# Kernel tuning notes

Measured on AMD Instinct MI355X. Metric: run time of the kernel, lower is better.

The kernel has to match this reference:

```python
import jax, jax.numpy as jnp
import numpy as np
import math

N_HEADS = 16
ROPE_BASE = 10000.0


def _rope_interleaved(t, cos, sin):
    # t: [B,H,T,dk]; cos/sin: [T, dk//2] broadcast over B,H
    te, to = t[..., 0::2], t[..., 1::2]
    re = te * cos - to * sin
    ro = te * sin + to * cos
    # interleave back: [..., dk//2, 2] -> [..., dk]
    return jnp.stack([re, ro], axis=-1).reshape(t.shape)


def setup_inputs() -> dict:
    key = jax.random.key(0)
    ks = jax.random.split(key, 5)
    B, T, C = 2, 2048, 1024
    s = 1.0 / math.sqrt(C)
    return {
        "x": jax.random.normal(ks[0], (B, T, C), dtype=jnp.float32),
        "W_qkv": jax.random.normal(ks[1], (C, 3 * C), dtype=jnp.float32) * s,
        "b_qkv": jax.random.normal(ks[2], (3 * C,), dtype=jnp.float32) * 0.02,
        "W_proj": jax.random.normal(ks[3], (C, C), dtype=jnp.float32) * s,
        "b_proj": jax.random.normal(ks[4], (C,), dtype=jnp.float32) * 0.02,
    }


def reference(x, W_qkv, b_qkv, W_proj, b_proj):
    B, T, C = x.shape
    H = N_HEADS
    dk = C // H

    qkv = x @ W_qkv + b_qkv                      # [B,T,3C]
    q, k, v = jnp.split(qkv, 3, axis=-1)
    q = q.reshape(B, T, H, dk).transpose(0, 2, 1, 3)  # [B,H,T,dk]
    k = k.reshape(B, T, H, dk).transpose(0, 2, 1, 3)
    v = v.reshape(B, T, H, dk).transpose(0, 2, 1, 3)

    # RoPE angles: pos * base^(-2i/dk)
    freqs = ROPE_BASE ** (-2.0 * jnp.arange(dk // 2, dtype=jnp.float32) / dk)
    angles = jnp.arange(T, dtype=jnp.float32)[:, None] * freqs[None, :]  # [T,dk//2]
    cos, sin = jnp.cos(angles), jnp.sin(angles)

    q = _rope_interleaved(q, cos, sin)
    k = _rope_interleaved(k, cos, sin)

    attn = jnp.einsum("bhqd,bhkd->bhqk", q, k) / math.sqrt(dk)  # [B,H,T,T]
    causal = jnp.triu(jnp.full((T, T), -jnp.inf, dtype=attn.dtype), k=1)
    attn = jax.nn.softmax(attn + causal, axis=-1)

    scores = jnp.einsum("bhqk,bhkd->bhqd", attn, v)  # [B,H,T,dk]
    scores = scores.transpose(0, 2, 1, 3).reshape(B, T, C)
    return scores @ W_proj + b_proj
```

## Files before the change

### kernel.cpp

```cpp
#include <hip/hip_runtime.h>
#include <hip/hip_bf16.h>

typedef __bf16 bf16x8 __attribute__((ext_vector_type(8)));
typedef float f32x4 __attribute__((ext_vector_type(4)));
typedef float f32x16 __attribute__((ext_vector_type(16)));
typedef unsigned short u16;
typedef u16 u16x8 __attribute__((ext_vector_type(8)));

__device__ __forceinline__ u16 f2bf(float f) {
  union { float f; unsigned u; } v; v.f = f;
  unsigned r = v.u + 0x7fffu + ((v.u >> 16) & 1u);
  return (u16)(r >> 16);
}
__device__ __forceinline__ float bf2f(u16 u) {
  union { unsigned u; float f; } v; v.u = (unsigned)u << 16; return v.f;
}
__device__ __forceinline__ unsigned cvtpk(float a, float b) {
  unsigned r;
  asm("v_cvt_pk_bf16_f32 %0, %1, %2" : "=v"(r) : "v"(a), "v"(b));
  return r;
}
__device__ __forceinline__ float exp2_(float x) {
  float r;
  asm("v_exp_f32 %0, %1" : "=v"(r) : "v"(x));
  return r;
}
__device__ __forceinline__ float sin2pi_(float x) {
  float r;
  asm("v_sin_f32 %0, %1" : "=v"(r) : "v"(x));
  return r;
}
__device__ __forceinline__ float cos2pi_(float x) {
  float r;
  asm("v_cos_f32 %0, %1" : "=v"(r) : "v"(x));
  return r;
}
__device__ __forceinline__ void gload16(const void* g, void* l) {
  __builtin_amdgcn_global_load_lds(
      (__attribute__((address_space(1))) void*)(void*)g,
      (__attribute__((address_space(3))) void*)l, 16, 0, 0);
}

union U8 { bf16x8 v; unsigned u[4]; };

__global__ __launch_bounds__(256) void cast_x_k(const float* __restrict__ x,
                                                u16* __restrict__ xb, int n8) {
  int id = blockIdx.x * 256 + threadIdx.x;
  if (id >= n8) return;
  const float4* p = (const float4*)(x + (size_t)id * 8);
  float4 a = p[0], b = p[1];
  u16x8 o;
  o[0] = f2bf(a.x); o[1] = f2bf(a.y); o[2] = f2bf(a.z); o[3] = f2bf(a.w);
  o[4] = f2bf(b.x); o[5] = f2bf(b.y); o[6] = f2bf(b.z); o[7] = f2bf(b.w);
  *(u16x8*)(xb + (size_t)id * 8) = o;
}

__global__ __launch_bounds__(256) void tcast_k(const float* __restrict__ W,
                                               u16* __restrict__ Wt, int R, int Cc) {
  __shared__ float tile[32][33];
  int bx = blockIdx.x * 32, by = blockIdx.y * 32;
  int tx = threadIdx.x & 31, ty = threadIdx.x >> 5;
#pragma unroll
  for (int j = 0; j < 4; j++)
    tile[ty + j * 8][tx] = W[(size_t)(by + ty + j * 8) * Cc + bx + tx];
  __syncthreads();
#pragma unroll
  for (int j = 0; j < 4; j++)
    Wt[(size_t)(bx + ty + j * 8) * R + by + tx] = f2bf(tile[tx][ty + j * 8]);
}

template <bool BF16OUT>
__global__ __launch_bounds__(256) void gemm_bt_k(const u16* __restrict__ A,
                                                 const u16* __restrict__ Bt,
                                                 const float* __restrict__ bias,
                                                 void* __restrict__ Cv,
                                                 int M, int N, int K) {
  __shared__ u16 As[128 * 64];
  __shared__ u16 Bs[128 * 64];
  int tid = threadIdx.x;
  int m0 = blockIdx.y * 128, n0 = blockIdx.x * 128;
  int wave = tid >> 6, lane = tid & 63;
  int wm = (wave & 1) * 64, wn = (wave >> 1) * 64;
  int lrow = lane & 15, lk = (lane >> 4) * 8;
  int rr = lane >> 3, cb = (lane & 7) * 16;

  f32x4 acc[4][4] = {};

  for (int k0 = 0; k0 < K; k0 += 64) {
#pragma unroll
    for (int i = 0; i < 4; i++) {
      int row = wave * 32 + i * 8 + rr;
      int cc = (cb ^ ((row & 7) << 4)) >> 1;
      gload16(A + (size_t)(m0 + row) * K + k0 + cc, &As[(wave * 32 + i * 8) * 64]);
      gload16(Bt + (size_t)(n0 + row) * K + k0 + cc, &Bs[(wave * 32 + i * 8) * 64]);
    }
    __syncthreads();
#pragma unroll
    for (int kk = 0; kk < 2; kk++) {
      bf16x8 af[4], bfr[4];
#pragma unroll
      for (int i = 0; i < 4; i++) {
        int arow = wm + i * 16 + lrow;
        int ab = (arow * 128 + (kk * 32 + lk) * 2) ^ ((arow & 7) << 4);
        af[i] = *(const bf16x8*)((const char*)As + ab);
        int brow = wn + i * 16 + lrow;
        int bb = (brow * 128 + (kk * 32 + lk) * 2) ^ ((brow & 7) << 4);
        bfr[i] = *(const bf16x8*)((const char*)Bs + bb);
      }
#pragma unroll
      for (int i = 0; i < 4; i++)
#pragma unroll
        for (int j = 0; j < 4; j++)
          acc[i][j] = __builtin_amdgcn_mfma_f32_16x16x32_bf16(af[i], bfr[j], acc[i][j], 0, 0, 0);
    }
    __syncthreads();
  }
  int rg = lane >> 4;
#pragma unroll
  for (int i = 0; i < 4; i++) {
#pragma unroll
    for (int j = 0; j < 4; j++) {
      int col = n0 + wn + j * 16 + lrow;
      float bz = bias ? bias[col] : 0.f;
#pragma unroll
      for (int r = 0; r < 4; r++) {
        int row = m0 + wm + i * 16 + rg * 4 + r;
        float val = acc[i][j][r] + bz;
        if constexpr (BF16OUT)
          ((u16*)Cv)[(size_t)row * N + col] = f2bf(val);
        else
          ((float*)Cv)[(size_t)row * N + col] = val;
      }
    }
  }
}

__global__ __launch_bounds__(256) void rope_pack_k(const u16* __restrict__ qkv,
                                                   u16* __restrict__ qf,
                                                   u16* __restrict__ kf,
                                                   u16* __restrict__ vf) {
  __shared__ u16 tl[64][72];
  int bh = blockIdx.x, tb = blockIdx.y;
  int b = bh >> 4, h = bh & 15;
  int tid = threadIdx.x;
  int tloc = tid >> 2;
  int a = tid & 3;
  int tg = tb * 64 + tloc;
  const u16* rowp = qkv + ((size_t)(b * 2048 + tg)) * 3072 + h * 64 + 16 * a;
  u16x8 q0 = *(const u16x8*)(rowp);
  u16x8 q1 = *(const u16x8*)(rowp + 8);
  u16x8 k0 = *(const u16x8*)(rowp + 1024);
  u16x8 k1 = *(const u16x8*)(rowp + 1032);
  const float QS = 0.18033688011112042f;
  const float C1 = -0.41524101186092029f;
  const float C2 = 0.15915494309189535f;
  u16x8 qo0, qo1, ko0, ko1;
#pragma unroll
  for (int j = 0; j < 8; j++) {
    int i = 8 * a + j;
    float fr = (float)tg * (exp2f((float)i * C1) * C2);
    fr = fr - floorf(fr);
    float sv = sin2pi_(fr), cv = cos2pi_(fr);
    float qx, qy, kx, ky;
    if (j < 4) {
      qx = bf2f(q0[2 * j]); qy = bf2f(q0[2 * j + 1]);
      kx = bf2f(k0[2 * j]); ky = bf2f(k0[2 * j + 1]);
    } else {
      qx = bf2f(q1[2 * j - 8]); qy = bf2f(q1[2 * j - 7]);
      kx = bf2f(k1[2 * j - 8]); ky = bf2f(k1[2 * j - 7]);
    }
    u16 qre = f2bf((qx * cv - qy * sv) * QS), qro = f2bf((qx * sv + qy * cv) * QS);
    u16 kre = f2bf(kx * cv - ky * sv),        kro = f2bf(kx * sv + ky * cv);
    if (j < 4) { qo0[2 * j] = qre; qo0[2 * j + 1] = qro; ko0[2 * j] = kre; ko0[2 * j + 1] = kro; }
    else       { qo1[2 * j - 8] = qre; qo1[2 * j - 7] = qro; ko1[2 * j - 8] = kre; ko1[2 * j - 7] = kro; }
  }
  size_t qbase = ((size_t)bh * 64 + (tg >> 5)) * 2048 + a * 512 + (tg & 31) * 8;
  *(u16x8*)(qf + qbase) = qo0;
  *(u16x8*)(qf + qbase + 256) = qo1;
  size_t kbase = (((size_t)bh * 32 + (tg >> 6)) * 2 + ((tg >> 5) & 1)) * 2048 + a * 512 + (tg & 31) * 8;
  *(u16x8*)(kf + kbase) = ko0;
  *(u16x8*)(kf + kbase + 256) = ko1;
#pragma unroll
  for (int rep = 0; rep < 2; rep++) {
    int tr = rep * 32 + (tid >> 3);
    int dc = (tid & 7) * 8;
    u16x8 v = *(const u16x8*)(qkv + ((size_t)(b * 2048 + tb * 64 + tr)) * 3072 + 2048 + h * 64 + dc);
    *(u16x8*)&tl[tr][dc] = v;
  }
  __syncthreads();
  u16* dst = vf + ((size_t)bh * 32 + tb) * 4096;
#pragma unroll
  for (int rep = 0; rep < 2; rep++) {
    int c = rep * 256 + tid;
    int dh = c >> 8, s = (c >> 6) & 3, l = c & 63;
    int hi = l >> 5, ql = l & 31;
    u16x8 o;
#pragma unroll
    for (int j = 0; j < 8; j++) o[j] = tl[s * 16 + hi * 8 + j][dh * 32 + ql];
    *(u16x8*)(dst + (size_t)c * 8) = o;
  }
}


#define KPREF(K0, K1, IT)                                                         \
  do {                                                                            \
    const u16* kb_ = KfP + (size_t)(IT) * 4096 + ln8;                             \
    _Pragma("unroll") for (int d_ = 0; d_ < 4; d_++) {                            \
      K0[d_] = *(const bf16x8*)(kb_ + d_ * 512);                                  \
      K1[d_] = *(const bf16x8*)(kb_ + 2048 + d_ * 512);                           \
    }                                                                             \
  } while (0)

#define QKC(SA, SB, K0, K1)                                                       \
  do {                                                                            \
    SA = (f32x16){};                                                              \
    SB = (f32x16){};                                                              \
    _Pragma("unroll") for (int d_ = 0; d_ < 4; d_++) {                            \
      SA = __builtin_amdgcn_mfma_f32_32x32x16_bf16(K0[d_], qfr[d_], SA, 0, 0, 0); \
      SB = __builtin_amdgcn_mfma_f32_32x32x16_bf16(K1[d_], qfr[d_], SB, 0, 0, 0); \
    }                                                                             \
  } while (0)

#define VLOADM(IT)                                                                \
  do {                                                                            \
    const u16* vb_ = VfP + (size_t)(IT) * 4096 + ln8;                             \
    _Pragma("unroll") for (int s_ = 0; s_ < 4; s_++) {                            \
      vv0[s_] = *(const bf16x8*)(vb_ + s_ * 512);                                 \
      vv1[s_] = *(const bf16x8*)(vb_ + 2048 + s_ * 512);                          \
    }                                                                             \
  } while (0)

#define SMPV(SA, SB, IT, MASKF)                                                   \
  do {                                                                            \
    if (MASKF) {                                                                  \
      int kv0_ = (IT) * 64;                                                       \
      _Pragma("unroll") for (int r_ = 0; r_ < 16; r_++) {                         \
        int ro_ = (r_ & 3) + 8 * (r_ >> 2) + 4 * hi;                              \
        if (kv0_ + ro_ > qg) SA[r_] = -3e38f;                                     \
        if (kv0_ + 32 + ro_ > qg) SB[r_] = -3e38f;                                \
      }                                                                           \
    }                                                                             \
    _Pragma("unroll") for (int r_ = 0; r_ < 16; r_++) {                           \
      SA[r_] = exp2_(SA[r_]);                                                     \
      SB[r_] = exp2_(SB[r_]);                                                     \
    }                                                                             \
    unsigned w0_ = cvtpk(SA[0], SA[1]),   w1_ = cvtpk(SA[2], SA[3]);              \
    unsigned w2_ = cvtpk(SA[4], SA[5]),   w3_ = cvtpk(SA[6], SA[7]);              \
    unsigned w4_ = cvtpk(SA[8], SA[9]),   w5_ = cvtpk(SA[10], SA[11]);            \
    unsigned w6_ = cvtpk(SA[12], SA[13]), w7_ = cvtpk(SA[14], SA[15]);            \
    unsigned y0_ = cvtpk(SB[0], SB[1]),   y1_ = cvtpk(SB[2], SB[3]);              \
    unsigned y2_ = cvtpk(SB[4], SB[5]),   y3_ = cvtpk(SB[6], SB[7]);              \
    unsigned y4_ = cvtpk(SB[8], SB[9]),   y5_ = cvtpk(SB[10], SB[11]);            \
    unsigned y6_ = cvtpk(SB[12], SB[13]), y7_ = cvtpk(SB[14], SB[15]);            \
    asm("v_permlane32_swap_b32 %0, %1" : "+v"(w0_), "+v"(w2_));                   \
    asm("v_permlane32_swap_b32 %0, %1" : "+v"(w1_), "+v"(w3_));                   \
    asm("v_permlane32_swap_b32 %0, %1" : "+v"(w4_), "+v"(w6_));                   \
    asm("v_permlane32_swap_b32 %0, %1" : "+v"(w5_), "+v"(w7_));                   \
    asm("v_permlane32_swap_b32 %0, %1" : "+v"(y0_), "+v"(y2_));                   \
    asm("v_permlane32_swap_b32 %0, %1" : "+v"(y1_), "+v"(y3_));                   \
    asm("v_permlane32_swap_b32 %0, %1" : "+v"(y4_), "+v"(y6_));                   \
    asm("v_permlane32_swap_b32 %0, %1" : "+v"(y5_), "+v"(y7_));                   \
    U8 pf0_, pf1_, pf2_, pf3_;                                                    \
    pf0_.u[0] = w0_; pf0_.u[1] = w1_; pf0_.u[2] = w2_; pf0_.u[3] = w3_;           \
    pf1_.u[0] = w4_; pf1_.u[1] = w5_; pf1_.u[2] = w6_; pf1_.u[3] = w7_;           \
    pf2_.u[0] = y0_; pf2_.u[1] = y1_; pf2_.u[2] = y2_; pf2_.u[3] = y3_;           \
    pf3_.u[0] = y4_; pf3_.u[1] = y5_; pf3_.u[2] = y6_; pf3_.u[3] = y7_;           \
    o0 = __builtin_amdgcn_mfma_f32_32x32x16_bf16(vv0[0], pf0_.v, o0, 0, 0, 0);    \
    o1 = __builtin_amdgcn_mfma_f32_32x32x16_bf16(vv1[0], pf0_.v, o1, 0, 0, 0);    \
    o0 = __builtin_amdgcn_mfma_f32_32x32x16_bf16(vv0[1], pf1_.v, o0, 0, 0, 0);    \
    o1 = __builtin_amdgcn_mfma_f32_32x32x16_bf16(vv1[1], pf1_.v, o1, 0, 0, 0);    \
    o0 = __builtin_amdgcn_mfma_f32_32x32x16_bf16(vv0[2], pf2_.v, o0, 0, 0, 0);    \
    o1 = __builtin_amdgcn_mfma_f32_32x32x16_bf16(vv1[2], pf2_.v, o1, 0, 0, 0);    \
    o0 = __builtin_amdgcn_mfma_f32_32x32x16_bf16(vv0[3], pf3_.v, o0, 0, 0, 0);    \
    o1 = __builtin_amdgcn_mfma_f32_32x32x16_bf16(vv1[3], pf3_.v, o1, 0, 0, 0);    \
    ls = __builtin_amdgcn_mfma_f32_32x32x16_bf16(onesf.v, pf0_.v, ls, 0, 0, 0);   \
    ls = __builtin_amdgcn_mfma_f32_32x32x16_bf16(onesf.v, pf1_.v, ls, 0, 0, 0);   \
    ls = __builtin_amdgcn_mfma_f32_32x32x16_bf16(onesf.v, pf2_.v, ls, 0, 0, 0);   \
    ls = __builtin_amdgcn_mfma_f32_32x32x16_bf16(onesf.v, pf3_.v, ls, 0, 0, 0);   \
  } while (0)

__global__ __launch_bounds__(64) void attn_k(const u16* __restrict__ Qf,
                                             const u16* __restrict__ Kf,
                                             const u16* __restrict__ Vf,
                                             u16* __restrict__ sc,
                                             u16* __restrict__ pO,
                                             float* __restrict__ pL) {
  const int T = 2048;
  int blk = blockIdx.x;
  int bh = (blk & 7) * 4 + ((blk >> 3) & 3);
  int c = blk >> 5;
  int qt, slot, nslots;
  if (c < 32) { qt = 63 - (c >> 1); slot = c & 1; nslots = 2; }
  else        { qt = 79 - c;        slot = 0;     nslots = 1; }
  int nTot = (qt >> 1) + 1;
  int it0 = (nTot * slot) / nslots;
  int itEnd = (nTot * (slot + 1)) / nslots;
  int lane = threadIdx.x & 63;
  int ql = lane & 31, hi = lane >> 5;
  int ln8 = lane * 8;
  int qg = qt * 32 + ql;
  const u16* QfP = Qf + (size_t)bh * 64 * 2048;
  const u16* KfP = Kf + (size_t)bh * 32 * 4096;
  const u16* VfP = Vf + (size_t)bh * 32 * 4096;
  int b = bh >> 4, h = bh & 15;

  U8 onesf;
#pragma unroll
  for (int j = 0; j < 4; j++) onesf.u[j] = 0x3F803F80u;

  bf16x8 qfr[4];
#pragma unroll
  for (int ds = 0; ds < 4; ds++)
    qfr[ds] = *(const bf16x8*)(QfP + (size_t)qt * 2048 + ds * 512 + ln8);

  f32x16 o0 = {}, o1 = {}, ls = {};
  bf16x8 Ka0[4], Ka1[4], Kb0[4], Kb1[4], vv0[4], vv1[4];
  f32x16 sA0, sA1, sB0, sB1;

  int t = it0;
  KPREF(Ka0, Ka1, t);
  QKC(sA0, sA1, Ka0, Ka1);
  if (t + 1 < itEnd) KPREF(Kb0, Kb1, t + 1);

  for (;;) {
    bool last = (t == itEnd - 1);
    VLOADM(t);
    if (t + 2 < itEnd) KPREF(Ka0, Ka1, t + 2);
    if (!last) QKC(sB0, sB1, Kb0, Kb1);
    SMPV(sA0, sA1, t, t == nTot - 1);
    if (last) break;
    ++t;
    last = (t == itEnd - 1);
    VLOADM(t);
    if (t + 2 < itEnd) KPREF(Kb0, Kb1, t + 2);
    if (!last) QKC(sA0, sA1, Ka0, Ka1);
    SMPV(sB0, sB1, t, t == nTot - 1);
    if (last) break;
    ++t;
  }

  if (nslots == 1) {
    float inv = 1.f / ls[0];
    u16* orow = sc + ((size_t)(b * T + qg)) * 1024 + h * 64;
#pragma unroll
    for (int j = 0; j < 4; j++) {
      ushort4 o;
      o.x = f2bf(o0[4 * j + 0] * inv); o.y = f2bf(o0[4 * j + 1] * inv);
      o.z = f2bf(o0[4 * j + 2] * inv); o.w = f2bf(o0[4 * j + 3] * inv);
      *(ushort4*)(orow + 8 * j + 4 * hi) = o;
      ushort4 q2;
      q2.x = f2bf(o1[4 * j + 0] * inv); q2.y = f2bf(o1[4 * j + 1] * inv);
      q2.z = f2bf(o1[4 * j + 2] * inv); q2.w = f2bf(o1[4 * j + 3] * inv);
      *(ushort4*)(orow + 32 + 8 * j + 4 * hi) = q2;
    }
  } else {
    u16* orow = pO + (size_t)slot * 4194304 + ((size_t)(b * T + qg)) * 1024 + h * 64;
#pragma unroll
    for (int j = 0; j < 4; j++) {
      ushort4 o;
      o.x = f2bf(o0[4 * j + 0]); o.y = f2bf(o0[4 * j + 1]);
      o.z = f2bf(o0[4 * j + 2]); o.w = f2bf(o0[4 * j + 3]);
      *(ushort4*)(orow + 8 * j + 4 * hi) = o;
      ushort4 q2;
      q2.x = f2bf(o1[4 * j + 0]); q2.y = f2bf(o1[4 * j + 1]);
      q2.z = f2bf(o1[4 * j + 2]); q2.w = f2bf(o1[4 * j + 3]);
      *(ushort4*)(orow + 32 + 8 * j + 4 * hi) = q2;
    }
    if (hi == 0) pL[slot * 65536 + bh * 2048 + qg] = ls[0];
  }
}

__global__ __launch_bounds__(256) void mrg_k(const u16* __restrict__ pO,
                                             const float* __restrict__ pL,
                                             u16* __restrict__ sc) {
  int id = blockIdx.x * 256 + threadIdx.x;
  int col8 = id & 127;
  int rp = id >> 7;
  int b = rp >> 9;
  int t = 1536 + (rp & 511);
  int h = col8 >> 3;
  int bh = b * 16 + h;
  size_t idx8 = ((size_t)(b * 2048 + t) * 128 + col8);
  float l0 = pL[bh * 2048 + t];
  float l1 = pL[65536 + bh * 2048 + t];
  u16x8 v0 = *(const u16x8*)(pO + idx8 * 8);
  u16x8 v1 = *(const u16x8*)(pO + 4194304 + idx8 * 8);
  float inv = 1.f / (l0 + l1);
  u16x8 o;
#pragma unroll
  for (int j = 0; j < 8; j++) o[j] = f2bf((bf2f(v0[j]) + bf2f(v1[j])) * inv);
  *(u16x8*)(sc + idx8 * 8) = o;
}

extern "C" void kernel_launch(void* const* d_in, const int* in_sizes, int n_in,
                              void* d_out, int out_size, void* d_ws, size_t ws_size,
                              hipStream_t stream) {
  const float* x      = (const float*)d_in[0];
  const float* W_qkv  = (const float*)d_in[1];
  const float* b_qkv  = (const float*)d_in[2];
  const float* W_proj = (const float*)d_in[3];
  const float* b_proj = (const float*)d_in[4];
  float* out = (float*)d_out;

  const int B = 2, T = 2048, C = 1024;
  const int M = B * T;

  char* ws = (char*)d_ws;
  u16* wprojt = (u16*)(ws);
  u16* xb     = (u16*)(ws + (2ull << 20));
  u16* wqkvt  = (u16*)(ws + (10ull << 20));
  u16* qkvb   = (u16*)(ws + (16ull << 20));
  u16* pO     = (u16*)(ws + (2ull << 20));
  float* pL   = (float*)(ws + (34ull << 20));
  u16* qfb    = (u16*)(ws + (40ull << 20));
  u16* kfb    = (u16*)(ws + (48ull << 20));
  u16* vfb    = (u16*)(ws + (56ull << 20));
  u16* sc     = (u16*)(ws + (64ull << 20));

  cast_x_k<<<(M * C / 8 + 255) / 256, 256, 0, stream>>>(x, xb, M * C / 8);
  tcast_k<<<dim3(3 * C / 32, C / 32), 256, 0, stream>>>(W_qkv, wqkvt, C, 3 * C);
  tcast_k<<<dim3(C / 32, C / 32), 256, 0, stream>>>(W_proj, wprojt, C, C);
  gemm_bt_k<true><<<dim3(3 * C / 128, M / 128), 256, 0, stream>>>(xb, wqkvt, b_qkv, qkvb, M, 3 * C, C);
  rope_pack_k<<<dim3(B * 16, T / 64), 256, 0, stream>>>(qkvb, qfb, kfb, vfb);
  attn_k<<<2560, 64, 0, stream>>>(qfb, kfb, vfb, sc, pO, pL);
  mrg_k<<<512, 256, 0, stream>>>(pO, pL, sc);
  gemm_bt_k<false><<<dim3(C / 128, M / 128), 256, 0, stream>>>(sc, wprojt, b_proj, out, M, C, C);
}
```

Before: 118.5 us.

## Fuse RoPE and Q/K/V repacking into QKV GEMM epilogue, merge weight casts

The QKV GEMM epilogue now applies bias, RoPE (using a precomputed cos/sin table and lane shuffles to pair even/odd columns) and writes Q, K, V directly in the attention kernel's packed layouts. This removes the bf16 qkv intermediate buffer and the separate rope_pack kernel. The two weight transpose-cast launches are merged into one kernel, and a small table kernel is added. In exchange, the epilogue issues scattered 2-byte stores and per-element table loads, which may be less coalesced than the old packing pass.

```diff
diff --git a/kernel.cpp b/kernel.cpp
--- a/kernel.cpp
+++ b/kernel.cpp
@@ -42,6 +42,16 @@
 }
 
 union U8 { bf16x8 v; unsigned u[4]; };
+
+__global__ __launch_bounds__(256) void ctab_k(float2* __restrict__ ctab) {
+  int id = blockIdx.x * 256 + threadIdx.x;
+  int t = id >> 5, i = id & 31;
+  const float C1 = -0.41524101186092029f;
+  const float C2 = 0.15915494309189535f;
+  float fr = (float)t * (exp2f((float)i * C1) * C2);
+  fr = fr - floorf(fr);
+  ctab[id] = make_float2(cos2pi_(fr), sin2pi_(fr));
+}
 
 __global__ __launch_bounds__(256) void cast_x_k(const float* __restrict__ x,
                                                 u16* __restrict__ xb, int n8) {
@@ -55,10 +65,17 @@
   *(u16x8*)(xb + (size_t)id * 8) = o;
 }
 
-__global__ __launch_bounds__(256) void tcast_k(const float* __restrict__ W,
-                                               u16* __restrict__ Wt, int R, int Cc) {
+__global__ __launch_bounds__(256) void tcast2_k(const float* __restrict__ Wq,
+                                                const float* __restrict__ Wp,
+                                                u16* __restrict__ Wqt,
+                                                u16* __restrict__ Wpt) {
   __shared__ float tile[32][33];
-  int bx = blockIdx.x * 32, by = blockIdx.y * 32;
+  int bxr = blockIdx.x;
+  const float* W; u16* Wt; int Cc, bx;
+  if (bxr < 96) { W = Wq; Wt = Wqt; Cc = 3072; bx = bxr * 32; }
+  else          { W = Wp; Wt = Wpt; Cc = 1024; bx = (bxr - 96) * 32; }
+  const int R = 1024;
+  int by = blockIdx.y * 32;
   int tx = threadIdx.x & 31, ty = threadIdx.x >> 5;
 #pragma unroll
   for (int j = 0; j < 4; j++)
@@ -135,72 +152,105 @@
   }
 }
 
-__global__ __launch_bounds__(256) void rope_pack_k(const u16* __restrict__ qkv,
+__global__ __launch_bounds__(256) void gemm_qkvf_k(const u16* __restrict__ A,
+                                                   const u16* __restrict__ Bt,
+                                                   const float* __restrict__ bias,
+                                                   const float2* __restrict__ ctab,
                                                    u16* __restrict__ qf,
                                                    u16* __restrict__ kf,
                                                    u16* __restrict__ vf) {
-  __shared__ u16 tl[64][72];
-  int bh = blockIdx.x, tb = blockIdx.y;
-  int b = bh >> 4, h = bh & 15;
+  const int K = 1024;
+  __shared__ u16 As[128 * 64];
+  __shared__ u16 Bs[128 * 64];
   int tid = threadIdx.x;
-  int tloc = tid >> 2;
-  int a = tid & 3;
-  int tg = tb * 64 + tloc;
-  const u16* rowp = qkv + ((size_t)(b * 2048 + tg)) * 3072 + h * 64 + 16 * a;
-  u16x8 q0 = *(const u16x8*)(rowp);
-  u16x8 q1 = *(const u16x8*)(rowp + 8);
-  u16x8 k0 = *(const u16x8*)(rowp + 1024);
-  u16x8 k1 = *(const u16x8*)(rowp + 1032);
+  int m0 = blockIdx.y * 128, n0 = blockIdx.x * 128;
+  int wave = tid >> 6, lane = tid & 63;
+  int wm = (wave & 1) * 64, wn = (wave >> 1) * 64;
+  int lrow = lane & 15, lk = (lane >> 4) * 8;
+  int rr = lane >> 3, cb = (lane & 7) * 16;
+
+  f32x4 acc[4][4] = {};
+
+  for (int k0 = 0; k0 < K; k0 += 64) {
+#pragma unroll
+    for (int i = 0; i < 4; i++) {
+      int row = wave * 32 + i * 8 + rr;
+      int cc = (cb ^ ((row & 7) << 4)) >> 1;
+      gload16(A + (size_t)(m0 + row) * K + k0 + cc, &As[(wave * 32 + i * 8) * 64]);
+      gload16(Bt + (size_t)(n0 + row) * K + k0 + cc, &Bs[(wave * 32 + i * 8) * 64]);
+    }
+    __syncthreads();
+#pragma unroll
+    for (int kk = 0; kk < 2; kk++) {
+      bf16x8 af[4], bfr[4];
+#pragma unroll
+      for (int i = 0; i < 4; i++) {
+        int arow = wm + i * 16 + lrow;
+        int ab = (arow * 128 + (kk * 32 + lk) * 2) ^ ((arow & 7) << 4);
+        af[i] = *(const bf16x8*)((const char*)As + ab);
+        int brow = wn + i * 16 + lrow;
+        int bb = (brow * 128 + (kk * 32 + lk) * 2) ^ ((brow & 7) << 4);
+        bfr[i] = *(const bf16x8*)((const char*)Bs + bb);
+      }
+#pragma unroll
+      for (int i = 0; i < 4; i++)
+#pragma unroll
+        for (int j = 0; j < 4; j++)
+          acc[i][j] = __builtin_amdgcn_mfma_f32_16x16x32_bf16(af[i], bfr[j], acc[i][j], 0, 0, 0);
+    }
+    __syncthreads();
+  }
+
+  int rg = lane >> 4;
+  int b = m0 >> 11, m0t = m0 & 2047;
+  int region = n0 >> 10;
   const float QS = 0.18033688011112042f;
-  const float C1 = -0.41524101186092029f;
-  const float C2 = 0.15915494309189535f;
-  u16x8 qo0, qo1, ko0, ko1;
-#pragma unroll
-  for (int j = 0; j < 8; j++) {
-    int i = 8 * a + j;
-    float fr = (float)tg * (exp2f((float)i * C1) * C2);
-    fr = fr - floorf(fr);
-    float sv = sin2pi_(fr), cv = cos2pi_(fr);
-    float qx, qy, kx, ky;
-    if (j < 4) {
-      qx = bf2f(q0[2 * j]); qy = bf2f(q0[2 * j + 1]);
-      kx = bf2f(k0[2 * j]); ky = bf2f(k0[2 * j + 1]);
-    } else {
-      qx = bf2f(q1[2 * j - 8]); qy = bf2f(q1[2 * j - 7]);
-      kx = bf2f(k1[2 * j - 8]); ky = bf2f(k1[2 * j - 7]);
-    }
-    u16 qre = f2bf((qx * cv - qy * sv) * QS), qro = f2bf((qx * sv + qy * cv) * QS);
-    u16 kre = f2bf(kx * cv - ky * sv),        kro = f2bf(kx * sv + ky * cv);
-    if (j < 4) { qo0[2 * j] = qre; qo0[2 * j + 1] = qro; ko0[2 * j] = kre; ko0[2 * j + 1] = kro; }
-    else       { qo1[2 * j - 8] = qre; qo1[2 * j - 7] = qro; ko1[2 * j - 8] = kre; ko1[2 * j - 7] = kro; }
-  }
-  size_t qbase = ((size_t)bh * 64 + (tg >> 5)) * 2048 + a * 512 + (tg & 31) * 8;
-  *(u16x8*)(qf + qbase) = qo0;
-  *(u16x8*)(qf + qbase + 256) = qo1;
-  size_t kbase = (((size_t)bh * 32 + (tg >> 6)) * 2 + ((tg >> 5) & 1)) * 2048 + a * 512 + (tg & 31) * 8;
-  *(u16x8*)(kf + kbase) = ko0;
-  *(u16x8*)(kf + kbase + 256) = ko1;
-#pragma unroll
-  for (int rep = 0; rep < 2; rep++) {
-    int tr = rep * 32 + (tid >> 3);
-    int dc = (tid & 7) * 8;
-    u16x8 v = *(const u16x8*)(qkv + ((size_t)(b * 2048 + tb * 64 + tr)) * 3072 + 2048 + h * 64 + dc);
-    *(u16x8*)&tl[tr][dc] = v;
-  }
-  __syncthreads();
-  u16* dst = vf + ((size_t)bh * 32 + tb) * 4096;
-#pragma unroll
-  for (int rep = 0; rep < 2; rep++) {
-    int c = rep * 256 + tid;
-    int dh = c >> 8, s = (c >> 6) & 3, l = c & 63;
-    int hi = l >> 5, ql = l & 31;
-    u16x8 o;
-#pragma unroll
-    for (int j = 0; j < 8; j++) o[j] = tl[s * 16 + hi * 8 + j][dh * 32 + ql];
-    *(u16x8*)(dst + (size_t)c * 8) = o;
-  }
-}
-
+  if (region < 2) {
+    u16* dstm = (region == 0) ? qf : kf;
+    float scale = (region == 0) ? QS : 1.0f;
+#pragma unroll
+    for (int j = 0; j < 4; j++) {
+      int colg = n0 + wn + j * 16 + lrow;
+      int de = colg & 63, h = (colg >> 6) & 15;
+      int ip = de >> 1, ds = de >> 4, hb = (de >> 3) & 1, j2 = de & 7;
+      float bz = bias[colg];
+      bool odd = (de & 1) != 0;
+      u16* dst = dstm + ((size_t)(b * 16 + h) * 64) * 2048 + ds * 512 + hb * 256 + j2;
+#pragma unroll
+      for (int i = 0; i < 4; i++) {
+#pragma unroll
+        for (int r = 0; r < 4; r++) {
+          int t = m0t + wm + i * 16 + rg * 4 + r;
+          float val = acc[i][j][r] + bz;
+          float pv = __shfl_xor(val, 1);
+          float2 cs = ctab[t * 32 + ip];
+          float outv = odd ? (pv * cs.y + val * cs.x) : (val * cs.x - pv * cs.y);
+          dst[(size_t)(t >> 5) * 2048 + (t & 31) * 8] = f2bf(outv * scale);
+        }
+      }
+    }
+  } else {
+#pragma unroll
+    for (int j = 0; j < 4; j++) {
+      int colg = n0 + wn + j * 16 + lrow;
+      int cv = colg - 2048, h = cv >> 6, dc = cv & 63;
+      float bz = bias[colg];
+      u16* dstb = vf + (size_t)(b * 16 + h) * 32 * 4096 + (dc >> 5) * 2048 +
+                  (dc & 31) * 8 + (rg & 1) * 4 + (rg >> 1) * 256;
+#pragma unroll
+      for (int i = 0; i < 4; i++) {
+        int tb = m0t + wm + i * 16;
+        size_t off = (size_t)(tb >> 6) * 4096 + (size_t)((tb & 63) >> 4) * 512;
+        ushort4 st;
+        st.x = f2bf(acc[i][j][0] + bz);
+        st.y = f2bf(acc[i][j][1] + bz);
+        st.z = f2bf(acc[i][j][2] + bz);
+        st.w = f2bf(acc[i][j][3] + bz);
+        *(ushort4*)(dstb + off) = st;
+      }
+    }
+  }
+}
 
 #define KPREF(K0, K1, IT)                                                         \
   do {                                                                            \
@@ -406,22 +456,21 @@
   const int M = B * T;
 
   char* ws = (char*)d_ws;
-  u16* wprojt = (u16*)(ws);
-  u16* xb     = (u16*)(ws + (2ull << 20));
-  u16* wqkvt  = (u16*)(ws + (10ull << 20));
-  u16* qkvb   = (u16*)(ws + (16ull << 20));
-  u16* pO     = (u16*)(ws + (2ull << 20));
-  float* pL   = (float*)(ws + (34ull << 20));
-  u16* qfb    = (u16*)(ws + (40ull << 20));
-  u16* kfb    = (u16*)(ws + (48ull << 20));
-  u16* vfb    = (u16*)(ws + (56ull << 20));
-  u16* sc     = (u16*)(ws + (64ull << 20));
-
+  u16* wprojt  = (u16*)(ws);
+  u16* xb      = (u16*)(ws + (2ull << 20));
+  u16* wqkvt   = (u16*)(ws + (10ull << 20));
+  u16* pO      = (u16*)(ws + (16ull << 20));
+  float* pL    = (float*)(ws + (32ull << 20));
+  float2* ctab = (float2*)(ws + (33ull << 20));
+  u16* qfb     = (u16*)(ws + (40ull << 20));
+  u16* kfb     = (u16*)(ws + (48ull << 20));
+  u16* vfb     = (u16*)(ws + (56ull << 20));
+  u16* sc      = (u16*)(ws + (64ull << 20));
+
+  ctab_k<<<256, 256, 0, stream>>>(ctab);
   cast_x_k<<<(M * C / 8 + 255) / 256, 256, 0, stream>>>(x, xb, M * C / 8);
-  tcast_k<<<dim3(3 * C / 32, C / 32), 256, 0, stream>>>(W_qkv, wqkvt, C, 3 * C);
-  tcast_k<<<dim3(C / 32, C / 32), 256, 0, stream>>>(W_proj, wprojt, C, C);
-  gemm_bt_k<true><<<dim3(3 * C / 128, M / 128), 256, 0, stream>>>(xb, wqkvt, b_qkv, qkvb, M, 3 * C, C);
-  rope_pack_k<<<dim3(B * 16, T / 64), 256, 0, stream>>>(qkvb, qfb, kfb, vfb);
+  tcast2_k<<<dim3(128, 32), 256, 0, stream>>>(W_qkv, W_proj, wqkvt, wprojt);
+  gemm_qkvf_k<<<dim3(3 * C / 128, M / 128), 256, 0, stream>>>(xb, wqkvt, b_qkv, ctab, qfb, kfb, vfb);
   attn_k<<<2560, 64, 0, stream>>>(qfb, kfb, vfb, sc, pO, pL);
   mrg_k<<<512, 256, 0, stream>>>(pO, pL, sc);
   gemm_bt_k<false><<<dim3(C / 128, M / 128), 256, 0, stream>>>(sc, wprojt, b_proj, out, M, C, C);
```

Measured after the change: 126.0 us. +6.3%, slower.
